# Kernel optimization log

Measured on AMD Instinct MI355X. Metric: run time of the kernel, lower is better.

## Reference

```python
import jax, jax.numpy as jnp
import numpy as np

ITERS = 8
LAMBDA0 = 0.01
PAD = 1.0
LR = 1.0
EPS = 1e-12


def _sobel_grads(fmap):
    # kornia spatial_gradient: normalized 3x3 sobel (/8), replicate padding. fmap: C,H,W
    kx = jnp.array([[-1., 0., 1.], [-2., 0., 2.], [-1., 0., 1.]], fmap.dtype) / 8.0
    k = jnp.stack([kx, kx.T])[:, None]                       # 2,1,3,3 (OIHW)
    f = jnp.pad(fmap, ((0, 0), (1, 1), (1, 1)), mode='edge')[:, None]  # C,1,H+2,W+2
    g = jax.lax.conv_general_dilated(f, k, (1, 1), 'VALID')  # C,2,H,W
    return g[:, 0], g[:, 1]


def _bilinear(tensor, pts):
    # grid_sample bilinear, align_corners=True, at pixel coords. tensor: C,H,W; pts: N,2 (x,y) -> N,C
    c, h, w = tensor.shape
    x, y = pts[:, 0], pts[:, 1]
    x0 = jnp.clip(jnp.floor(x), 0, w - 1)
    y0 = jnp.clip(jnp.floor(y), 0, h - 1)
    x1 = jnp.clip(x0 + 1, 0, w - 1)
    y1 = jnp.clip(y0 + 1, 0, h - 1)
    wx, wy = x - x0, y - y0
    x0i, x1i = x0.astype(jnp.int32), x1.astype(jnp.int32)
    y0i, y1i = y0.astype(jnp.int32), y1.astype(jnp.int32)
    v00 = tensor[:, y0i, x0i]
    v01 = tensor[:, y0i, x1i]
    v10 = tensor[:, y1i, x0i]
    v11 = tensor[:, y1i, x1i]
    out = (v00 * (1 - wx) * (1 - wy) + v01 * wx * (1 - wy)
           + v10 * (1 - wx) * wy + v11 * wx * wy)
    return out.T


def _skew(v):
    x, y, z = v[..., 0], v[..., 1], v[..., 2]
    o = jnp.zeros_like(x)
    return jnp.stack([o, -z, y, z, o, -x, -y, x, o], -1).reshape(v.shape[:-1] + (3, 3))


def _so3exp(w):
    theta = jnp.linalg.norm(w)
    small = theta < 1e-7
    th = jnp.where(small, 1.0, theta)
    A = jnp.where(small, 1.0, jnp.sin(th) / th)
    B = jnp.where(small, 0.5, (1.0 - jnp.cos(th)) / th ** 2)
    W = _skew(w)
    return jnp.eye(3, dtype=w.dtype) + A * W + B * (W @ W)


def _normalize(x):
    return x / jnp.maximum(jnp.linalg.norm(x, axis=-1, keepdims=True), EPS)


def _pnp(p3D, feature_ref, feature_query, K, R_init, t_init):
    C, H, W = feature_query.shape
    gx, gy = _sobel_grads(feature_query)
    fref = _normalize(feature_ref)
    fx, fy, cx, cy = K[0, 0], K[1, 1], K[0, 2], K[1, 2]
    f_scale = jnp.stack([fx, fy])
    c_off = jnp.stack([cx, cy])

    def project(R, t):
        p3q = p3D @ R.T + t
        pn = p3q[:, :2] / p3q[:, 2:3]
        return p3q, pn, pn * f_scale + c_off

    def in_image(p2):
        return ((p2[:, 0] >= PAD) & (p2[:, 0] < W - PAD)
                & (p2[:, 1] >= PAD) & (p2[:, 1] < H - PAD))

    def masked_cost(p2, vf):
        f = _normalize(_bilinear(feature_query, p2))
        cost = ((f - fref) ** 2).sum(-1)
        return (cost * vf).sum() / vf.sum()

    R, t = R_init, t_init
    lam = jnp.asarray(LAMBDA0, p3D.dtype)
    jacobi = None
    cost_best = None
    p2D_init = None

    for i in range(ITERS):
        p3q, pn, p2 = project(R, t)
        if i == 0:
            p2D_init = jax.lax.stop_gradient(p2)
        vf = in_image(p2).astype(p3D.dtype)  # mask-weight == gather of valid pts

        f_raw = _bilinear(feature_query, p2)  # N,C
        norm = jnp.maximum(jnp.linalg.norm(f_raw, axis=-1, keepdims=True), EPS)
        f = f_raw / norm
        error = f - fref
        if i == 0:
            cost_best = (((error ** 2).sum(-1)) * vf).sum() / vf.sum()

        # Jacobian chain: J = J_f_p2 @ J_p2_pn @ J_pn_p3 @ J_p3_T   -> N,C,6
        x_, y_, d = p3q[:, 0], p3q[:, 1], p3q[:, 2]
        z = jnp.zeros_like(d)
        Jpn = jnp.stack([1 / d, z, -x_ / d ** 2,
                         z, 1 / d, -y_ / d ** 2], -1).reshape(-1, 2, 3)
        Jpn = Jpn * f_scale[None, :, None]  # fold in J_p2_pn = diag(fx,fy)
        Jp3T = jnp.concatenate(
            [jnp.broadcast_to(jnp.eye(3, dtype=p3D.dtype), p3q.shape[:-1] + (3, 3)),
             -_skew(p3q)], -1)  # N,3,6
        J26 = Jpn @ Jp3T       # N,2,6

        Jf = jnp.stack([_bilinear(gx, p2), _bilinear(gy, p2)], -1)  # N,C,2
        # normalize-feat Jacobian (I - f f^T)/||f_raw||, fused (no NxCxC)
        proj = jnp.einsum('nc,nck->nk', f, Jf)
        Jf = (Jf - f[:, :, None] * proj[:, None, :]) / norm[:, :, None]

        J = Jf @ J26  # N,C,6
        if i == 0:
            jacobi = 1.0 / (1.0 + jnp.linalg.norm(J * vf[:, None, None], axis=(0, 1)))
        J = J * jacobi

        Grad = jnp.einsum('ncj,nc,n->j', J, error, vf)
        Hess = jnp.einsum('nci,ncj,n->ij', J, J, vf)

        damp = jnp.diag(jnp.diagonal(Hess) + 1e-9) * lam  # LM damping
        delta = -LR * jnp.linalg.solve(Hess + damp, Grad)
        delta = delta * jacobi
        dt, dw = delta[:3], delta[3:6]
        dr = _so3exp(dw)
        R_new, t_new = dr @ R, dr @ t + dt

        _, _, p2_new = project(R_new, t_new)
        vf_new = in_image(p2_new).astype(p3D.dtype)
        cost_new = masked_cost(p2_new, vf_new)

        accept = cost_new <= cost_best
        lam = jnp.clip(lam * jnp.where(accept, 0.1, 10.0), 1e-8, 1e4)
        R = jnp.where(accept, R_new, R)
        t = jnp.where(accept, t_new, t)
        cost_best = jnp.where(accept, cost_new, cost_best)

    p3D_sg = jax.lax.stop_gradient(p3D)
    pf = p3D_sg @ R.T + t
    p2f = (pf[:, :2] / pf[:, 2:3]) * f_scale + c_off
    f_i = _normalize(_bilinear(feature_query, p2D_init))
    f_f = _normalize(_bilinear(feature_query, p2f))
    cost_init = ((fref - f_i) ** 2).sum(-1)
    cost_final = ((fref - f_f) ** 2).sum(-1)
    nan = jnp.asarray(jnp.nan, cost_init.dtype)
    cost_init = jnp.where(in_image(p2D_init), cost_init, nan)
    cost_final = jnp.where(in_image(p2f), cost_final, nan)
    return R, t, cost_init, cost_final


def setup_inputs() -> dict:
    N, C, H, W = 10000, 128, 512, 512
    key = jax.random.key(0)
    ks = jax.random.split(key, 4)
    xy = jax.random.uniform(ks[0], (N, 2), jnp.float32, -2.0, 2.0)
    z = jax.random.uniform(ks[1], (N, 1), jnp.float32, 4.0, 10.0)
    p3D = jnp.concatenate([xy, z], -1)
    feature_query = jax.random.normal(ks[2], (C, H, W), jnp.float32) * 0.5
    feature_ref = jax.random.normal(ks[3], (N, C), jnp.float32)
    K = jnp.array([[500., 0., 256.], [0., 500., 256.], [0., 0., 1.]], jnp.float32)
    R_init = _so3exp(jnp.array([0.01, -0.02, 0.015], jnp.float32))
    t_init = jnp.array([0.05, -0.03, 0.10], jnp.float32)
    return {"p3D": p3D, "feature_ref": feature_ref, "feature_query": feature_query,
            "K": K, "R_init": R_init, "t_init": t_init}


def reference(p3D, feature_ref, feature_query, K, R_init, t_init):
    return _pnp(p3D, feature_ref, feature_query, K, R_init, t_init)
```

## Files before the change

### kernel.cpp

```cpp
#include <hip/hip_runtime.h>
#include <hip/hip_fp16.h>
#include <math.h>

#define HW_ (512*512)

typedef float vf4 __attribute__((ext_vector_type(4)));

__device__ __forceinline__ float wred(float v){
#pragma unroll
  for (int o = 32; o > 0; o >>= 1) v += __shfl_xor(v, o, 64);
  return v;
}

template<bool TR>
__device__ __forceinline__ float2 tap(const void* __restrict__ f, int y, int x, int c0){
  if (TR){
    const __half2* p = (const __half2*)f + (((size_t)((y << 9) + x)) << 6) + (c0 >> 1);
    return __half22float2(*p);
  } else {
    const float* ff = (const float*)f;
    int base = (y << 9) + x;
    float2 r;
    r.x = ff[(size_t)c0 * HW_ + base];
    r.y = ff[(size_t)(c0 + 1) * HW_ + base];
    return r;
  }
}

template<bool TR>
__device__ __forceinline__ float cost_point_raw(const void* __restrict__ fmap,
                                                const float* __restrict__ fref,
                                                int n, float px, float py, int lane){
  int c0 = 2 * lane;
  float x0f = fminf(fmaxf(floorf(px), 0.f), 511.f);
  float y0f = fminf(fmaxf(floorf(py), 0.f), 511.f);
  int x0 = (int)x0f, y0 = (int)y0f;
  int x1 = min(x0 + 1, 511), y1 = min(y0 + 1, 511);
  float wx = px - x0f, wy = py - y0f;
  float w00 = (1.f-wx)*(1.f-wy), w01 = wx*(1.f-wy), w10 = (1.f-wx)*wy, w11 = wx*wy;
  float2 a = tap<TR>(fmap, y0, x0, c0), b = tap<TR>(fmap, y0, x1, c0);
  float2 c = tap<TR>(fmap, y1, x0, c0), d = tap<TR>(fmap, y1, x1, c0);
  float f0 = w00*a.x + w01*b.x + w10*c.x + w11*d.x;
  float f1 = w00*a.y + w01*b.y + w10*c.y + w11*d.y;
  const float2 fr = *(const float2*)(fref + (size_t)n*128 + c0);
  float Sff  = wred(f0*f0 + f1*f1);
  float Sffr = wred(f0*fr.x + f1*fr.y);
  float Sfr  = wred(fr.x*fr.x + fr.y*fr.y);
  float inv = 1.f / fmaxf(sqrtf(Sff), 1e-12f);
  float irn = 1.f / fmaxf(sqrtf(Sfr), 1e-12f);
  return Sff*inv*inv - 2.f*Sffr*inv*irn + Sfr*irn*irn;
}

__global__ __launch_bounds__(512) void transpose_kernel(const float* __restrict__ fq,
                                                        __half* __restrict__ ftr,
                                                        double* __restrict__ cur2){
  __shared__ __half tile[256 * 128];
  int t = threadIdx.x;
  if (blockIdx.x == 0 && t < 256) cur2[t] = 0.0;
  int sb = blockIdx.x << 8;
  int l = t & 63, r = t >> 6;
  int px0 = l << 2;
#pragma unroll
  for (int p = 0; p < 16; p++){
    int ch = p * 8 + r;
    vf4 v = __builtin_nontemporal_load((const vf4*)(fq + (size_t)ch * HW_ + sb + px0));
#pragma unroll
    for (int j = 0; j < 4; j++){
      int px = px0 + j;
      tile[px * 128 + (ch ^ (px & 0x78))] = __float2half(v[j]);
    }
  }
  __syncthreads();
#pragma unroll
  for (int p = 0; p < 8; p++){
    int px = p * 32 + (t >> 4);
    int c8 = (t & 15) << 3;
    int cs = c8 ^ (px & 0x78);
    uint4 v = *(const uint4*)&tile[px * 128 + cs];
    *(uint4*)(ftr + ((size_t)(sb + px) << 7) + c8) = v;
  }
}

__global__ void init_kernel(double* __restrict__ cur2){
  if (threadIdx.x < 256) cur2[threadIdx.x] = 0.0;
}

template<bool TR>
__device__ __forceinline__ bool gather_pt(
    const float* __restrict__ p3D, const float* __restrict__ fref,
    const void* __restrict__ fmap, const float* Rl, const float* Tl,
    float fx, float fy, float cx, float cy,
    int n, int lane, float s[10], float& X, float& Y, float& D)
{
  float PX = p3D[3*n], PY = p3D[3*n+1], PZ = p3D[3*n+2];
  X = Rl[0]*PX + Rl[1]*PY + Rl[2]*PZ + Tl[0];
  Y = Rl[3]*PX + Rl[4]*PY + Rl[5]*PZ + Tl[1];
  D = Rl[6]*PX + Rl[7]*PY + Rl[8]*PZ + Tl[2];
  float px = X / D * fx + cx;
  float py = Y / D * fy + cy;
  if (!(px >= 1.f && px < 511.f && py >= 1.f && py < 511.f)) return false;
  int c0 = 2 * lane;
  float x0f = fminf(fmaxf(floorf(px), 0.f), 511.f);
  float y0f = fminf(fmaxf(floorf(py), 0.f), 511.f);
  int x0 = (int)x0f, y0 = (int)y0f;
  int x1 = min(x0 + 1, 511), y1 = min(y0 + 1, 511);
  float wx = px - x0f, wy = py - y0f;
  int xs0 = max(x0-1,0), xs3 = min(x1+1,511);
  int ys0 = max(y0-1,0), ys3 = min(y1+1,511);
  float ea = (1.f-wx)*(1.f-wy), eb = wx*(1.f-wy), ec = (1.f-wx)*wy, ed = wx*wy;
  float a8 = 0.125f*ea, b8 = 0.125f*eb, c8 = 0.125f*ec, d8 = 0.125f*ed;
  float gL1 = 2.f*a8 + c8, gR1 = 2.f*b8 + d8;
  float gL2 = a8 + 2.f*c8, gR2 = b8 + 2.f*d8;
  float ya0 = a8, ya1 = 2.f*a8 + b8, ya2 = a8 + 2.f*b8, ya3 = b8;
  float yc0 = c8, yc1 = 2.f*c8 + d8, yc2 = c8 + 2.f*d8, yc3 = d8;
  float f0=0.f, f1=0.f, gx0=0.f, gx1=0.f, gy0=0.f, gy1=0.f;
  float2 t0, t1, t2, t3;
  t0 = tap<TR>(fmap, ys0, xs0, c0); t1 = tap<TR>(fmap, ys0, x0, c0);
  t2 = tap<TR>(fmap, ys0, x1,  c0); t3 = tap<TR>(fmap, ys0, xs3, c0);
  gx0 += a8*(t2.x-t0.x) + b8*(t3.x-t1.x);
  gx1 += a8*(t2.y-t0.y) + b8*(t3.y-t1.y);
  gy0 -= ya0*t0.x + ya1*t1.x + ya2*t2.x + ya3*t3.x;
  gy1 -= ya0*t0.y + ya1*t1.y + ya2*t2.y + ya3*t3.y;
  t0 = tap<TR>(fmap, y0, xs0, c0); t1 = tap<TR>(fmap, y0, x0, c0);
  t2 = tap<TR>(fmap, y0, x1,  c0); t3 = tap<TR>(fmap, y0, xs3, c0);
  gx0 += gL1*(t2.x-t0.x) + gR1*(t3.x-t1.x);
  gx1 += gL1*(t2.y-t0.y) + gR1*(t3.y-t1.y);
  gy0 -= yc0*t0.x + yc1*t1.x + yc2*t2.x + yc3*t3.x;
  gy1 -= yc0*t0.y + yc1*t1.y + yc2*t2.y + yc3*t3.y;
  f0 += ea*t1.x + eb*t2.x;  f1 += ea*t1.y + eb*t2.y;
  t0 = tap<TR>(fmap, y1, xs0, c0); t1 = tap<TR>(fmap, y1, x0, c0);
  t2 = tap<TR>(fmap, y1, x1,  c0); t3 = tap<TR>(fmap, y1, xs3, c0);
  gx0 += gL2*(t2.x-t0.x) + gR2*(t3.x-t1.x);
  gx1 += gL2*(t2.y-t0.y) + gR2*(t3.y-t1.y);
  gy0 += ya0*t0.x + ya1*t1.x + ya2*t2.x + ya3*t3.x;
  gy1 += ya0*t0.y + ya1*t1.y + ya2*t2.y + ya3*t3.y;
  f0 += ec*t1.x + ed*t2.x;  f1 += ec*t1.y + ed*t2.y;
  t0 = tap<TR>(fmap, ys3, xs0, c0); t1 = tap<TR>(fmap, ys3, x0, c0);
  t2 = tap<TR>(fmap, ys3, x1,  c0); t3 = tap<TR>(fmap, ys3, xs3, c0);
  gx0 += c8*(t2.x-t0.x) + d8*(t3.x-t1.x);
  gx1 += c8*(t2.y-t0.y) + d8*(t3.y-t1.y);
  gy0 += yc0*t0.x + yc1*t1.x + yc2*t2.x + yc3*t3.x;
  gy1 += yc0*t0.y + yc1*t1.y + yc2*t2.y + yc3*t3.y;
  const float2 fr = *(const float2*)(fref + (size_t)n*128 + c0);
  s[0] = f0*f0 + f1*f1;
  s[1] = f0*fr.x + f1*fr.y;
  s[2] = fr.x*fr.x + fr.y*fr.y;
  s[3] = f0*gx0 + f1*gx1;
  s[4] = f0*gy0 + f1*gy1;
  s[5] = gx0*fr.x + gx1*fr.y;
  s[6] = gy0*fr.x + gy1*fr.y;
  s[7] = gx0*gx0 + gx1*gx1;
  s[8] = gx0*gy0 + gx1*gy1;
  s[9] = gy0*gy0 + gy1*gy1;
  return true;
}

__device__ __forceinline__ float slot_val(const float s[10], float X, float Y, float D,
                                          float fx, float fy, int lane, int li, int lj,
                                          float& se2)
{
  float inv = 1.f / fmaxf(sqrtf(s[0]), 1e-12f);
  float irn = 1.f / fmaxf(sqrtf(s[2]), 1e-12f);
  float inv2 = inv*inv, inv3 = inv2*inv, inv4 = inv2*inv2;
  float Sffr = s[1]*irn, Sgxfr = s[5]*irn, Sgyfr = s[6]*irn, Sfr = s[2]*irn*irn;
  se2 = s[0]*inv2 - 2.f*Sffr*inv + Sfr;
  float gex = s[3]*inv2 - Sgxfr*inv - s[3]*s[0]*inv4 + s[3]*Sffr*inv3;
  float gey = s[4]*inv2 - Sgyfr*inv - s[4]*s[0]*inv4 + s[4]*Sffr*inv3;
  float sxx = s[7]*inv2 - s[3]*s[3]*inv4;
  float sxy = s[8]*inv2 - s[3]*s[4]*inv4;
  float syy = s[9]*inv2 - s[4]*s[4]*inv4;
  float invD = 1.f / D;
  float rx = X * invD, ry = Y * invD;
  float A[6] = {fx*invD, 0.f, -fx*rx*invD, -fx*rx*ry, fx*(1.f+rx*rx), -fx*ry};
  float B[6] = {0.f, fy*invD, -fy*ry*invD, -fy*(1.f+ry*ry), fy*rx*ry, fy*rx};
  float val = 0.f;
  if (lane < 6)        val = A[lane]*gex + B[lane]*gey;
  else if (lane < 27)  val = A[li]*A[lj]*sxx + (A[li]*B[lj] + A[lj]*B[li])*sxy + B[li]*B[lj]*syy;
  else if (lane == 27) val = se2;
  else if (lane == 28) val = 1.f;
  return val;
}

template<bool TR>
__global__ __launch_bounds__(256) void eval_kernel(
    const float* __restrict__ p3D, const float* __restrict__ fref,
    const void* __restrict__ fmap, const float* __restrict__ Km,
    const float* __restrict__ Rm, const float* __restrict__ tm,
    const float* __restrict__ state, double* __restrict__ cur2,
    float* __restrict__ costT, float* __restrict__ costF,
    float* __restrict__ costI, int N, int mode)
{
  int t = threadIdx.x, lane = t & 63, wv = t >> 6;
  int gw = blockIdx.x * 4 + wv;
  int nw = (gridDim.x * blockDim.x) >> 6;
  if (mode == 1 && state[32] != 0.f){
    int nn = gw + lane * nw;
    if (lane < 4 && nn < N) costF[nn] = costT[nn];
  }
  float fx = Km[0], fy = Km[4], cx = Km[2], cy = Km[5];
  float Rl[9], Tl[3];
#pragma unroll
  for (int i = 0; i < 9; i++) Rl[i] = Rm[i];
#pragma unroll
  for (int i = 0; i < 3; i++) Tl[i] = tm[i];
  int li = 0, lj = 0;
  {
    const int pi_[21] = {0,0,0,0,0,0,1,1,1,1,1,2,2,2,2,3,3,3,4,4,5};
    const int pj_[21] = {0,1,2,3,4,5,1,2,3,4,5,2,3,4,5,3,4,5,4,5,5};
    if (lane >= 6 && lane < 27){ li = pi_[lane-6]; lj = pj_[lane-6]; }
  }
  const float nanv = __int_as_float(0x7fc00000);
  double acc = 0.0;
  for (int n = gw; n < N; n += nw){
    float s[10], X, Y, D;
    bool v = gather_pt<TR>(p3D, fref, fmap, Rl, Tl, fx, fy, cx, cy, n, lane, s, X, Y, D);
    float se2 = 0.f;
    if (v){
#pragma unroll
      for (int i = 0; i < 10; i++) s[i] = wred(s[i]);
      acc += (double)slot_val(s, X, Y, D, fx, fy, lane, li, lj, se2);
    }
    if (lane == 0){
      float cv = v ? se2 : nanv;
      if (mode == 0){ costI[n] = cv; costF[n] = cv; }
      else costT[n] = cv;
    }
  }
  __shared__ double red[4][32];
  if (lane < 32) red[wv][lane] = acc;
  __syncthreads();
  if (t < 32){
    double ssum = red[0][t] + red[1][t] + red[2][t] + red[3][t];
    if (ssum != 0.0) atomicAdd(&cur2[t*8 + (blockIdx.x & 7)], ssum);
  }
}

template<bool TR>
__global__ __launch_bounds__(256) void cost_kernel(
    const float* __restrict__ p3D, const float* __restrict__ fref,
    const void* __restrict__ fmap, const float* __restrict__ Km,
    const float* __restrict__ Rm, const float* __restrict__ tm,
    const float* __restrict__ state, double* __restrict__ cur2,
    float* __restrict__ costT, float* __restrict__ costF, int N)
{
  int t = threadIdx.x, lane = t & 63, wv = t >> 6;
  int gw = blockIdx.x * 4 + wv;
  int nw = (gridDim.x * blockDim.x) >> 6;
  if (state[32] != 0.f){
    int nn = gw + lane * nw;
    if (lane < 4 && nn < N) costF[nn] = costT[nn];
  }
  float fx = Km[0], fy = Km[4], cx = Km[2], cy = Km[5];
  float Rl[9], Tl[3];
#pragma unroll
  for (int i = 0; i < 9; i++) Rl[i] = Rm[i];
#pragma unroll
  for (int i = 0; i < 3; i++) Tl[i] = tm[i];
  const float nanv = __int_as_float(0x7fc00000);
  double accc = 0.0, accn = 0.0;
  for (int n = gw; n < N; n += nw){
    float PX = p3D[3*n], PY = p3D[3*n+1], PZ = p3D[3*n+2];
    float X = Rl[0]*PX + Rl[1]*PY + Rl[2]*PZ + Tl[0];
    float Y = Rl[3]*PX + Rl[4]*PY + Rl[5]*PZ + Tl[1];
    float D = Rl[6]*PX + Rl[7]*PY + Rl[8]*PZ + Tl[2];
    float px = X / D * fx + cx, py = Y / D * fy + cy;
    bool v = (px >= 1.f && px < 511.f && py >= 1.f && py < 511.f);
    float cp = 0.f;
    if (v){ cp = cost_point_raw<TR>(fmap, fref, n, px, py, lane); accc += (double)cp; accn += 1.0; }
    if (lane == 0) costT[n] = v ? cp : nanv;
  }
  double acc = (lane == 27) ? accc : ((lane == 28) ? accn : 0.0);
  __shared__ double red[4][32];
  if (lane < 32) red[wv][lane] = acc;
  __syncthreads();
  if (t < 32){
    double ssum = red[0][t] + red[1][t] + red[2][t] + red[3][t];
    if (ssum != 0.0) atomicAdd(&cur2[t*8 + (blockIdx.x & 7)], ssum);
  }
}

__device__ void solve_step(const double* __restrict__ cur, float* __restrict__ state){
  const int pi_[21] = {0,0,0,0,0,0,1,1,1,1,1,2,2,2,2,3,3,3,4,4,5};
  const int pj_[21] = {0,1,2,3,4,5,1,2,3,4,5,2,3,4,5,3,4,5,4,5,5};
  double rg[6]; for (int i = 0; i < 6; i++) rg[i] = cur[i];
  double rh[6][6];
  for (int k = 0; k < 21; k++){ rh[pi_[k]][pj_[k]] = cur[6+k]; rh[pj_[k]][pi_[k]] = cur[6+k]; }
  float jac[6];
  for (int j = 0; j < 6; j++) jac[j] = state[24+j];
  double lam = (double)state[30];
  double H[6][7];
  for (int i = 0; i < 6; i++)
    for (int j = 0; j < 6; j++) H[i][j] = (double)jac[i] * (double)jac[j] * rh[i][j];
  for (int i = 0; i < 6; i++) H[i][i] += (H[i][i] + 1e-9) * lam;
  for (int i = 0; i < 6; i++) H[i][6] = -((double)jac[i] * rg[i]);
  for (int k = 0; k < 6; k++){
    int p = k; double mx = fabs(H[k][k]);
    for (int r = k+1; r < 6; r++) if (fabs(H[r][k]) > mx){ mx = fabs(H[r][k]); p = r; }
    if (p != k) for (int c = k; c < 7; c++){ double tmp = H[k][c]; H[k][c] = H[p][c]; H[p][c] = tmp; }
    double inv = 1.0 / H[k][k];
    for (int r = k+1; r < 6; r++){
      double m = H[r][k] * inv;
      for (int c = k; c < 7; c++) H[r][c] -= m * H[k][c];
    }
  }
  double d[6];
  for (int i = 5; i >= 0; i--){
    double sx = H[i][6];
    for (int c = i+1; c < 6; c++) sx -= H[i][c] * d[c];
    d[i] = sx / H[i][i];
  }
  for (int j = 0; j < 6; j++) d[j] *= (double)jac[j];
  double wx = d[3], wy = d[4], wz = d[5];
  double th2 = wx*wx + wy*wy + wz*wz, th = sqrt(th2);
  double Aa, Bb;
  if (th < 1e-7){ Aa = 1.0; Bb = 0.5; } else { Aa = sin(th)/th; Bb = (1.0 - cos(th))/th2; }
  double W[3][3] = {{0,-wz,wy},{wz,0,-wx},{-wy,wx,0}};
  double W2[3][3];
  for (int i = 0; i < 3; i++) for (int j = 0; j < 3; j++){
    double q = 0; for (int k = 0; k < 3; k++) q += W[i][k]*W[k][j]; W2[i][j] = q;
  }
  double dr[3][3];
  for (int i = 0; i < 3; i++) for (int j = 0; j < 3; j++)
    dr[i][j] = (i == j ? 1.0 : 0.0) + Aa*W[i][j] + Bb*W2[i][j];
  double Rc[3][3], tc[3];
  for (int i = 0; i < 3; i++){ tc[i] = state[9+i]; for (int j = 0; j < 3; j++) Rc[i][j] = state[i*3+j]; }
  for (int i = 0; i < 3; i++){
    for (int j = 0; j < 3; j++){
      double q = 0; for (int k = 0; k < 3; k++) q += dr[i][k]*Rc[k][j];
      state[12 + i*3 + j] = (float)q;
    }
    double q = 0; for (int k = 0; k < 3; k++) q += dr[i][k]*tc[k];
    state[21 + i] = (float)(q + d[i]);
  }
}

__global__ void update_kernel(double* __restrict__ cur2, float* __restrict__ state,
                              double* __restrict__ cur,
                              const float* __restrict__ Rin, const float* __restrict__ tin,
                              int iter)
{
  __shared__ double tot[32];
  int t = threadIdx.x;
  if (t < 32){
    double s = 0.0;
#pragma unroll
    for (int k = 0; k < 8; k++){ s += cur2[t*8 + k]; cur2[t*8 + k] = 0.0; }
    tot[t] = s;
  }
  __syncthreads();
  if (t != 0) return;
  if (iter < 0){
    for (int i = 0; i < 9; i++) state[i] = Rin[i];
    for (int i = 0; i < 3; i++) state[9+i] = tin[i];
    state[30] = 0.01f;
    state[32] = 0.f;
    const int diag_k[6] = {0, 6, 11, 15, 18, 20};
    for (int j = 0; j < 6; j++)
      state[24+j] = 1.0f / (1.0f + (float)sqrt(tot[6 + diag_k[j]]));
    state[31] = (float)(tot[27] / tot[28]);
    for (int k = 0; k < 32; k++) cur[k] = tot[k];
    solve_step(cur, state);
  } else {
    float cn = (float)(tot[27] / tot[28]);
    bool acpt = (cn <= state[31]);
    float lam = state[30] * (acpt ? 0.1f : 10.f);
    state[30] = fminf(fmaxf(lam, 1e-8f), 1e4f);
    state[32] = acpt ? 1.f : 0.f;
    if (acpt){
      for (int i = 0; i < 12; i++) state[i] = state[12+i];
      state[31] = cn;
      for (int k = 0; k < 32; k++) cur[k] = tot[k];
    }
    if (iter < 7) solve_step(cur, state);
  }
}

__global__ __launch_bounds__(256) void final_kernel(const float* __restrict__ state,
                                                    const float* __restrict__ costT,
                                                    float* __restrict__ out, int N)
{
  int g = blockIdx.x * blockDim.x + threadIdx.x;
  if (g < 12) out[g] = state[g];
  if (state[32] != 0.f){
    int stride = gridDim.x * blockDim.x;
    for (int n = g; n < N; n += stride) out[12 + N + n] = costT[n];
  }
}

extern "C" void kernel_launch(void* const* d_in, const int* in_sizes, int n_in,
                              void* d_out, int out_size, void* d_ws, size_t ws_size,
                              hipStream_t stream)
{
  const float* p3D  = (const float*)d_in[0];
  const float* fref = (const float*)d_in[1];
  const float* fq   = (const float*)d_in[2];
  const float* Km   = (const float*)d_in[3];
  const float* Rin  = (const float*)d_in[4];
  const float* tin  = (const float*)d_in[5];
  float* out = (float*)d_out;
  int N = in_sizes[0] / 3;
  const int EBLK = 1024;

  char* w = (char*)d_ws;
  float*  state = (float*)w;
  double* cur   = (double*)(w + 256);
  double* cur2  = (double*)(w + 512);
  float*  costT = (float*)(w + 2560);
  size_t ftr_off = (2560 + (size_t)N*4 + 255) & ~(size_t)255;
  __half* ftr = (__half*)(w + ftr_off);
  size_t need = ftr_off + (size_t)HW_ * 128 * 2;
  bool tr = (ws_size >= need);

  float* costI = out + 12;
  float* costF = out + 12 + N;

  if (tr) transpose_kernel<<<HW_/256, 512, 0, stream>>>(fq, ftr, cur2);
  else    init_kernel<<<1, 256, 0, stream>>>(cur2);
  const void* fmap = tr ? (const void*)ftr : (const void*)fq;

  if (tr) eval_kernel<true ><<<EBLK, 256, 0, stream>>>(p3D, fref, fmap, Km, Rin, tin, state, cur2, costT, costF, costI, N, 0);
  else    eval_kernel<false><<<EBLK, 256, 0, stream>>>(p3D, fref, fmap, Km, Rin, tin, state, cur2, costT, costF, costI, N, 0);
  update_kernel<<<1, 64, 0, stream>>>(cur2, state, cur, Rin, tin, -1);

  for (int it = 0; it < 7; it++){
    if (tr) eval_kernel<true ><<<EBLK, 256, 0, stream>>>(p3D, fref, fmap, Km, state + 12, state + 21, state, cur2, costT, costF, nullptr, N, 1);
    else    eval_kernel<false><<<EBLK, 256, 0, stream>>>(p3D, fref, fmap, Km, state + 12, state + 21, state, cur2, costT, costF, nullptr, N, 1);
    update_kernel<<<1, 64, 0, stream>>>(cur2, state, cur, Rin, tin, it);
  }
  if (tr) cost_kernel<true ><<<EBLK, 256, 0, stream>>>(p3D, fref, fmap, Km, state + 12, state + 21, state, cur2, costT, costF, N);
  else    cost_kernel<false><<<EBLK, 256, 0, stream>>>(p3D, fref, fmap, Km, state + 12, state + 21, state, cur2, costT, costF, N);
  update_kernel<<<1, 64, 0, stream>>>(cur2, state, cur, Rin, tin, 7);

  final_kernel<<<256, 256, 0, stream>>>(state, costT, out, N);
}
```

Before: 533.4 us.

## Map one wavefront per point with 512-thread blocks and batch 4x4 tap loads

The eval and cost kernels now launch one wavefront per 3D point with 8 waves per block, replacing the grid-stride loop over 1024 blocks. The 16 neighbourhood taps are loaded into register arrays up front, and the Sobel gradient plus bilinear value are computed from that patch. The goal is more memory parallelism, since all gathers can be issued before any arithmetic, and better load balance. In exchange, each iteration launches many more blocks, doing more atomic adds into the reduction slots, and register pressure rises from holding 32 tap values.

```diff
diff --git a/kernel.cpp b/kernel.cpp
--- a/kernel.cpp
+++ b/kernel.cpp
@@ -25,6 +25,21 @@
     r.y = ff[(size_t)(c0 + 1) * HW_ + base];
     return r;
   }
+}
+
+__device__ __forceinline__ void fgrad(const float P[16], float w00, float w01, float w10, float w11,
+                                      float& f, float& gx, float& gy){
+  f = w00*P[5] + w01*P[6] + w10*P[9] + w11*P[10];
+  float gx11 = (P[2]  + 2.f*P[6]  + P[10] - P[0] - 2.f*P[4]  - P[8] ) * 0.125f;
+  float gx12 = (P[3]  + 2.f*P[7]  + P[11] - P[1] - 2.f*P[5]  - P[9] ) * 0.125f;
+  float gx21 = (P[6]  + 2.f*P[10] + P[14] - P[4] - 2.f*P[8]  - P[12]) * 0.125f;
+  float gx22 = (P[7]  + 2.f*P[11] + P[15] - P[5] - 2.f*P[9]  - P[13]) * 0.125f;
+  gx = w00*gx11 + w01*gx12 + w10*gx21 + w11*gx22;
+  float gy11 = (P[8]  + 2.f*P[9]  + P[10] - P[0] - 2.f*P[1]  - P[2] ) * 0.125f;
+  float gy12 = (P[9]  + 2.f*P[10] + P[11] - P[1] - 2.f*P[2]  - P[3] ) * 0.125f;
+  float gy21 = (P[12] + 2.f*P[13] + P[14] - P[4] - 2.f*P[5]  - P[6] ) * 0.125f;
+  float gy22 = (P[13] + 2.f*P[14] + P[15] - P[5] - 2.f*P[6]  - P[7] ) * 0.125f;
+  gy = w00*gy11 + w01*gy12 + w10*gy21 + w11*gy22;
 }
 
 template<bool TR>
@@ -86,103 +101,7 @@
 }
 
 template<bool TR>
-__device__ __forceinline__ bool gather_pt(
-    const float* __restrict__ p3D, const float* __restrict__ fref,
-    const void* __restrict__ fmap, const float* Rl, const float* Tl,
-    float fx, float fy, float cx, float cy,
-    int n, int lane, float s[10], float& X, float& Y, float& D)
-{
-  float PX = p3D[3*n], PY = p3D[3*n+1], PZ = p3D[3*n+2];
-  X = Rl[0]*PX + Rl[1]*PY + Rl[2]*PZ + Tl[0];
-  Y = Rl[3]*PX + Rl[4]*PY + Rl[5]*PZ + Tl[1];
-  D = Rl[6]*PX + Rl[7]*PY + Rl[8]*PZ + Tl[2];
-  float px = X / D * fx + cx;
-  float py = Y / D * fy + cy;
-  if (!(px >= 1.f && px < 511.f && py >= 1.f && py < 511.f)) return false;
-  int c0 = 2 * lane;
-  float x0f = fminf(fmaxf(floorf(px), 0.f), 511.f);
-  float y0f = fminf(fmaxf(floorf(py), 0.f), 511.f);
-  int x0 = (int)x0f, y0 = (int)y0f;
-  int x1 = min(x0 + 1, 511), y1 = min(y0 + 1, 511);
-  float wx = px - x0f, wy = py - y0f;
-  int xs0 = max(x0-1,0), xs3 = min(x1+1,511);
-  int ys0 = max(y0-1,0), ys3 = min(y1+1,511);
-  float ea = (1.f-wx)*(1.f-wy), eb = wx*(1.f-wy), ec = (1.f-wx)*wy, ed = wx*wy;
-  float a8 = 0.125f*ea, b8 = 0.125f*eb, c8 = 0.125f*ec, d8 = 0.125f*ed;
-  float gL1 = 2.f*a8 + c8, gR1 = 2.f*b8 + d8;
-  float gL2 = a8 + 2.f*c8, gR2 = b8 + 2.f*d8;
-  float ya0 = a8, ya1 = 2.f*a8 + b8, ya2 = a8 + 2.f*b8, ya3 = b8;
-  float yc0 = c8, yc1 = 2.f*c8 + d8, yc2 = c8 + 2.f*d8, yc3 = d8;
-  float f0=0.f, f1=0.f, gx0=0.f, gx1=0.f, gy0=0.f, gy1=0.f;
-  float2 t0, t1, t2, t3;
-  t0 = tap<TR>(fmap, ys0, xs0, c0); t1 = tap<TR>(fmap, ys0, x0, c0);
-  t2 = tap<TR>(fmap, ys0, x1,  c0); t3 = tap<TR>(fmap, ys0, xs3, c0);
-  gx0 += a8*(t2.x-t0.x) + b8*(t3.x-t1.x);
-  gx1 += a8*(t2.y-t0.y) + b8*(t3.y-t1.y);
-  gy0 -= ya0*t0.x + ya1*t1.x + ya2*t2.x + ya3*t3.x;
-  gy1 -= ya0*t0.y + ya1*t1.y + ya2*t2.y + ya3*t3.y;
-  t0 = tap<TR>(fmap, y0, xs0, c0); t1 = tap<TR>(fmap, y0, x0, c0);
-  t2 = tap<TR>(fmap, y0, x1,  c0); t3 = tap<TR>(fmap, y0, xs3, c0);
-  gx0 += gL1*(t2.x-t0.x) + gR1*(t3.x-t1.x);
-  gx1 += gL1*(t2.y-t0.y) + gR1*(t3.y-t1.y);
-  gy0 -= yc0*t0.x + yc1*t1.x + yc2*t2.x + yc3*t3.x;
-  gy1 -= yc0*t0.y + yc1*t1.y + yc2*t2.y + yc3*t3.y;
-  f0 += ea*t1.x + eb*t2.x;  f1 += ea*t1.y + eb*t2.y;
-  t0 = tap<TR>(fmap, y1, xs0, c0); t1 = tap<TR>(fmap, y1, x0, c0);
-  t2 = tap<TR>(fmap, y1, x1,  c0); t3 = tap<TR>(fmap, y1, xs3, c0);
-  gx0 += gL2*(t2.x-t0.x) + gR2*(t3.x-t1.x);
-  gx1 += gL2*(t2.y-t0.y) + gR2*(t3.y-t1.y);
-  gy0 += ya0*t0.x + ya1*t1.x + ya2*t2.x + ya3*t3.x;
-  gy1 += ya0*t0.y + ya1*t1.y + ya2*t2.y + ya3*t3.y;
-  f0 += ec*t1.x + ed*t2.x;  f1 += ec*t1.y + ed*t2.y;
-  t0 = tap<TR>(fmap, ys3, xs0, c0); t1 = tap<TR>(fmap, ys3, x0, c0);
-  t2 = tap<TR>(fmap, ys3, x1,  c0); t3 = tap<TR>(fmap, ys3, xs3, c0);
-  gx0 += c8*(t2.x-t0.x) + d8*(t3.x-t1.x);
-  gx1 += c8*(t2.y-t0.y) + d8*(t3.y-t1.y);
-  gy0 += yc0*t0.x + yc1*t1.x + yc2*t2.x + yc3*t3.x;
-  gy1 += yc0*t0.y + yc1*t1.y + yc2*t2.y + yc3*t3.y;
-  const float2 fr = *(const float2*)(fref + (size_t)n*128 + c0);
-  s[0] = f0*f0 + f1*f1;
-  s[1] = f0*fr.x + f1*fr.y;
-  s[2] = fr.x*fr.x + fr.y*fr.y;
-  s[3] = f0*gx0 + f1*gx1;
-  s[4] = f0*gy0 + f1*gy1;
-  s[5] = gx0*fr.x + gx1*fr.y;
-  s[6] = gy0*fr.x + gy1*fr.y;
-  s[7] = gx0*gx0 + gx1*gx1;
-  s[8] = gx0*gy0 + gx1*gy1;
-  s[9] = gy0*gy0 + gy1*gy1;
-  return true;
-}
-
-__device__ __forceinline__ float slot_val(const float s[10], float X, float Y, float D,
-                                          float fx, float fy, int lane, int li, int lj,
-                                          float& se2)
-{
-  float inv = 1.f / fmaxf(sqrtf(s[0]), 1e-12f);
-  float irn = 1.f / fmaxf(sqrtf(s[2]), 1e-12f);
-  float inv2 = inv*inv, inv3 = inv2*inv, inv4 = inv2*inv2;
-  float Sffr = s[1]*irn, Sgxfr = s[5]*irn, Sgyfr = s[6]*irn, Sfr = s[2]*irn*irn;
-  se2 = s[0]*inv2 - 2.f*Sffr*inv + Sfr;
-  float gex = s[3]*inv2 - Sgxfr*inv - s[3]*s[0]*inv4 + s[3]*Sffr*inv3;
-  float gey = s[4]*inv2 - Sgyfr*inv - s[4]*s[0]*inv4 + s[4]*Sffr*inv3;
-  float sxx = s[7]*inv2 - s[3]*s[3]*inv4;
-  float sxy = s[8]*inv2 - s[3]*s[4]*inv4;
-  float syy = s[9]*inv2 - s[4]*s[4]*inv4;
-  float invD = 1.f / D;
-  float rx = X * invD, ry = Y * invD;
-  float A[6] = {fx*invD, 0.f, -fx*rx*invD, -fx*rx*ry, fx*(1.f+rx*rx), -fx*ry};
-  float B[6] = {0.f, fy*invD, -fy*ry*invD, -fy*(1.f+ry*ry), fy*rx*ry, fy*rx};
-  float val = 0.f;
-  if (lane < 6)        val = A[lane]*gex + B[lane]*gey;
-  else if (lane < 27)  val = A[li]*A[lj]*sxx + (A[li]*B[lj] + A[lj]*B[li])*sxy + B[li]*B[lj]*syy;
-  else if (lane == 27) val = se2;
-  else if (lane == 28) val = 1.f;
-  return val;
-}
-
-template<bool TR>
-__global__ __launch_bounds__(256) void eval_kernel(
+__global__ __launch_bounds__(512) void eval_kernel(
     const float* __restrict__ p3D, const float* __restrict__ fref,
     const void* __restrict__ fmap, const float* __restrict__ Km,
     const float* __restrict__ Rm, const float* __restrict__ tm,
@@ -190,92 +109,146 @@
     float* __restrict__ costT, float* __restrict__ costF,
     float* __restrict__ costI, int N, int mode)
 {
-  int t = threadIdx.x, lane = t & 63, wv = t >> 6;
-  int gw = blockIdx.x * 4 + wv;
-  int nw = (gridDim.x * blockDim.x) >> 6;
+  int t = threadIdx.x;
+  int lane = t & 63;
+  int wv = t >> 6;
+  int n = blockIdx.x * 8 + wv;
   if (mode == 1 && state[32] != 0.f){
-    int nn = gw + lane * nw;
-    if (lane < 4 && nn < N) costF[nn] = costT[nn];
-  }
-  float fx = Km[0], fy = Km[4], cx = Km[2], cy = Km[5];
-  float Rl[9], Tl[3];
-#pragma unroll
-  for (int i = 0; i < 9; i++) Rl[i] = Rm[i];
-#pragma unroll
-  for (int i = 0; i < 3; i++) Tl[i] = tm[i];
-  int li = 0, lj = 0;
-  {
-    const int pi_[21] = {0,0,0,0,0,0,1,1,1,1,1,2,2,2,2,3,3,3,4,4,5};
-    const int pj_[21] = {0,1,2,3,4,5,1,2,3,4,5,2,3,4,5,3,4,5,4,5,5};
-    if (lane >= 6 && lane < 27){ li = pi_[lane-6]; lj = pj_[lane-6]; }
-  }
-  const float nanv = __int_as_float(0x7fc00000);
+    int gid = blockIdx.x * 512 + t;
+    if (gid < N) costF[gid] = costT[gid];
+  }
   double acc = 0.0;
-  for (int n = gw; n < N; n += nw){
-    float s[10], X, Y, D;
-    bool v = gather_pt<TR>(p3D, fref, fmap, Rl, Tl, fx, fy, cx, cy, n, lane, s, X, Y, D);
+  if (n < N){
+    float fx = Km[0], fy = Km[4], cx = Km[2], cy = Km[5];
+    float R0=Rm[0],R1=Rm[1],R2=Rm[2],R3=Rm[3],R4=Rm[4];
+    float R5=Rm[5],R6=Rm[6],R7=Rm[7],R8=Rm[8];
+    float t0=tm[0], t1=tm[1], t2=tm[2];
+    float PX = p3D[3*n], PY = p3D[3*n+1], PZ = p3D[3*n+2];
+    float X = R0*PX + R1*PY + R2*PZ + t0;
+    float Y = R3*PX + R4*PY + R5*PZ + t1;
+    float D = R6*PX + R7*PY + R8*PZ + t2;
+    float px = X / D * fx + cx;
+    float py = Y / D * fy + cy;
+    bool valid = (px >= 1.f && px < 511.f && py >= 1.f && py < 511.f);
     float se2 = 0.f;
-    if (v){
-#pragma unroll
-      for (int i = 0; i < 10; i++) s[i] = wred(s[i]);
-      acc += (double)slot_val(s, X, Y, D, fx, fy, lane, li, lj, se2);
+    if (valid){
+      int c0 = 2 * lane;
+      float x0f = fminf(fmaxf(floorf(px), 0.f), 511.f);
+      float y0f = fminf(fmaxf(floorf(py), 0.f), 511.f);
+      int x0 = (int)x0f, y0 = (int)y0f;
+      int x1 = min(x0 + 1, 511), y1 = min(y0 + 1, 511);
+      float wx = px - x0f, wy = py - y0f;
+      int xs[4] = {max(x0-1,0), x0, x1, min(x1+1,511)};
+      int ys[4] = {max(y0-1,0), y0, y1, min(y1+1,511)};
+      float Pa[16], Pb[16];
+#pragma unroll
+      for (int r = 0; r < 4; r++)
+#pragma unroll
+        for (int sc = 0; sc < 4; sc++){
+          float2 v = tap<TR>(fmap, ys[r], xs[sc], c0);
+          Pa[r*4+sc] = v.x; Pb[r*4+sc] = v.y;
+        }
+      float w00 = (1.f-wx)*(1.f-wy), w01 = wx*(1.f-wy), w10 = (1.f-wx)*wy, w11 = wx*wy;
+      float f0, gx0, gy0, f1, gx1, gy1;
+      fgrad(Pa, w00, w01, w10, w11, f0, gx0, gy0);
+      fgrad(Pb, w00, w01, w10, w11, f1, gx1, gy1);
+      const float2 fr2 = *(const float2*)(fref + (size_t)n*128 + c0);
+      float Sff   = wred(f0*f0   + f1*f1);
+      float Sffr0 = wred(f0*fr2.x + f1*fr2.y);
+      float Sfr   = wred(fr2.x*fr2.x + fr2.y*fr2.y);
+      float Sfgx  = wred(f0*gx0  + f1*gx1);
+      float Sfgy  = wred(f0*gy0  + f1*gy1);
+      float Sgxf0 = wred(gx0*fr2.x + gx1*fr2.y);
+      float Sgyf0 = wred(gy0*fr2.x + gy1*fr2.y);
+      float Sgxgx = wred(gx0*gx0 + gx1*gx1);
+      float Sgxgy = wred(gx0*gy0 + gx1*gy1);
+      float Sgygy = wred(gy0*gy0 + gy1*gy1);
+      float irn = 1.f / fmaxf(sqrtf(Sfr), 1e-12f);
+      float Sffr = Sffr0*irn, Sgxfr = Sgxf0*irn, Sgyfr = Sgyf0*irn, Sfrn = Sfr*irn*irn;
+      float nrm = fmaxf(sqrtf(Sff), 1e-12f);
+      float inv = 1.f/nrm, inv2 = inv*inv, inv3 = inv2*inv, inv4 = inv2*inv2;
+      se2 = Sff*inv2 - 2.f*Sffr*inv + Sfrn;
+      float gex = Sfgx*inv2 - Sgxfr*inv - Sfgx*Sff*inv4 + Sfgx*Sffr*inv3;
+      float gey = Sfgy*inv2 - Sgyfr*inv - Sfgy*Sff*inv4 + Sfgy*Sffr*inv3;
+      float sxx = Sgxgx*inv2 - Sfgx*Sfgx*inv4;
+      float sxy = Sgxgy*inv2 - Sfgx*Sfgy*inv4;
+      float syy = Sgygy*inv2 - Sfgy*Sfgy*inv4;
+      float invD = 1.f / D;
+      float rx = X * invD, ry = Y * invD;
+      float A[6] = {fx*invD, 0.f, -fx*rx*invD, -fx*rx*ry, fx*(1.f+rx*rx), -fx*ry};
+      float B[6] = {0.f, fy*invD, -fy*ry*invD, -fy*(1.f+ry*ry), fy*rx*ry, fy*rx};
+      int li = 0, lj = 0;
+      {
+        const int pi_[21] = {0,0,0,0,0,0,1,1,1,1,1,2,2,2,2,3,3,3,4,4,5};
+        const int pj_[21] = {0,1,2,3,4,5,1,2,3,4,5,2,3,4,5,3,4,5,4,5,5};
+        if (lane >= 6 && lane < 27){ li = pi_[lane-6]; lj = pj_[lane-6]; }
+      }
+      float val = 0.f;
+      if (lane < 6)        val = A[lane]*gex + B[lane]*gey;
+      else if (lane < 27)  val = A[li]*A[lj]*sxx + (A[li]*B[lj] + A[lj]*B[li])*sxy + B[li]*B[lj]*syy;
+      else if (lane == 27) val = se2;
+      else if (lane == 28) val = 1.f;
+      acc = (double)val;
     }
     if (lane == 0){
-      float cv = v ? se2 : nanv;
+      float cv = valid ? se2 : __int_as_float(0x7fc00000);
       if (mode == 0){ costI[n] = cv; costF[n] = cv; }
       else costT[n] = cv;
     }
   }
-  __shared__ double red[4][32];
+  __shared__ double red[8][32];
   if (lane < 32) red[wv][lane] = acc;
   __syncthreads();
   if (t < 32){
-    double ssum = red[0][t] + red[1][t] + red[2][t] + red[3][t];
-    if (ssum != 0.0) atomicAdd(&cur2[t*8 + (blockIdx.x & 7)], ssum);
+    double s = 0.0;
+#pragma unroll
+    for (int i = 0; i < 8; i++) s += red[i][t];
+    if (s != 0.0) atomicAdd(&cur2[t*8 + (blockIdx.x & 7)], s);
   }
 }
 
 template<bool TR>
-__global__ __launch_bounds__(256) void cost_kernel(
+__global__ __launch_bounds__(512) void cost_kernel(
     const float* __restrict__ p3D, const float* __restrict__ fref,
     const void* __restrict__ fmap, const float* __restrict__ Km,
     const float* __restrict__ Rm, const float* __restrict__ tm,
     const float* __restrict__ state, double* __restrict__ cur2,
     float* __restrict__ costT, float* __restrict__ costF, int N)
 {
-  int t = threadIdx.x, lane = t & 63, wv = t >> 6;
-  int gw = blockIdx.x * 4 + wv;
-  int nw = (gridDim.x * blockDim.x) >> 6;
+  int t = threadIdx.x;
+  int lane = t & 63;
+  int wv = t >> 6;
+  int n = blockIdx.x * 8 + wv;
   if (state[32] != 0.f){
-    int nn = gw + lane * nw;
-    if (lane < 4 && nn < N) costF[nn] = costT[nn];
-  }
-  float fx = Km[0], fy = Km[4], cx = Km[2], cy = Km[5];
-  float Rl[9], Tl[3];
-#pragma unroll
-  for (int i = 0; i < 9; i++) Rl[i] = Rm[i];
-#pragma unroll
-  for (int i = 0; i < 3; i++) Tl[i] = tm[i];
-  const float nanv = __int_as_float(0x7fc00000);
-  double accc = 0.0, accn = 0.0;
-  for (int n = gw; n < N; n += nw){
+    int gid = blockIdx.x * 512 + t;
+    if (gid < N) costF[gid] = costT[gid];
+  }
+  double acc = 0.0;
+  bool valid = false;
+  float cp = 0.f;
+  if (n < N){
+    float fx = Km[0], fy = Km[4], cx = Km[2], cy = Km[5];
     float PX = p3D[3*n], PY = p3D[3*n+1], PZ = p3D[3*n+2];
-    float X = Rl[0]*PX + Rl[1]*PY + Rl[2]*PZ + Tl[0];
-    float Y = Rl[3]*PX + Rl[4]*PY + Rl[5]*PZ + Tl[1];
-    float D = Rl[6]*PX + Rl[7]*PY + Rl[8]*PZ + Tl[2];
+    float X = Rm[0]*PX + Rm[1]*PY + Rm[2]*PZ + tm[0];
+    float Y = Rm[3]*PX + Rm[4]*PY + Rm[5]*PZ + tm[1];
+    float D = Rm[6]*PX + Rm[7]*PY + Rm[8]*PZ + tm[2];
     float px = X / D * fx + cx, py = Y / D * fy + cy;
-    bool v = (px >= 1.f && px < 511.f && py >= 1.f && py < 511.f);
-    float cp = 0.f;
-    if (v){ cp = cost_point_raw<TR>(fmap, fref, n, px, py, lane); accc += (double)cp; accn += 1.0; }
-    if (lane == 0) costT[n] = v ? cp : nanv;
-  }
-  double acc = (lane == 27) ? accc : ((lane == 28) ? accn : 0.0);
-  __shared__ double red[4][32];
+    valid = (px >= 1.f && px < 511.f && py >= 1.f && py < 511.f);
+    if (valid) cp = cost_point_raw<TR>(fmap, fref, n, px, py, lane);
+    if (lane == 0) costT[n] = valid ? cp : __int_as_float(0x7fc00000);
+    if (valid){
+      if (lane == 27) acc = (double)cp;
+      else if (lane == 28) acc = 1.0;
+    }
+  }
+  __shared__ double red[8][32];
   if (lane < 32) red[wv][lane] = acc;
   __syncthreads();
   if (t < 32){
-    double ssum = red[0][t] + red[1][t] + red[2][t] + red[3][t];
-    if (ssum != 0.0) atomicAdd(&cur2[t*8 + (blockIdx.x & 7)], ssum);
+    double s = 0.0;
+#pragma unroll
+    for (int i = 0; i < 8; i++) s += red[i][t];
+    if (s != 0.0) atomicAdd(&cur2[t*8 + (blockIdx.x & 7)], s);
   }
 }
 
@@ -399,7 +372,7 @@
   const float* tin  = (const float*)d_in[5];
   float* out = (float*)d_out;
   int N = in_sizes[0] / 3;
-  const int EBLK = 1024;
+  int NBLK = (N + 7) / 8;
 
   char* w = (char*)d_ws;
   float*  state = (float*)w;
@@ -418,17 +391,17 @@
   else    init_kernel<<<1, 256, 0, stream>>>(cur2);
   const void* fmap = tr ? (const void*)ftr : (const void*)fq;
 
-  if (tr) eval_kernel<true ><<<EBLK, 256, 0, stream>>>(p3D, fref, fmap, Km, Rin, tin, state, cur2, costT, costF, costI, N, 0);
-  else    eval_kernel<false><<<EBLK, 256, 0, stream>>>(p3D, fref, fmap, Km, Rin, tin, state, cur2, costT, costF, costI, N, 0);
+  if (tr) eval_kernel<true ><<<NBLK, 512, 0, stream>>>(p3D, fref, fmap, Km, Rin, tin, state, cur2, costT, costF, costI, N, 0);
+  else    eval_kernel<false><<<NBLK, 512, 0, stream>>>(p3D, fref, fmap, Km, Rin, tin, state, cur2, costT, costF, costI, N, 0);
   update_kernel<<<1, 64, 0, stream>>>(cur2, state, cur, Rin, tin, -1);
 
   for (int it = 0; it < 7; it++){
-    if (tr) eval_kernel<true ><<<EBLK, 256, 0, stream>>>(p3D, fref, fmap, Km, state + 12, state + 21, state, cur2, costT, costF, nullptr, N, 1);
-    else    eval_kernel<false><<<EBLK, 256, 0, stream>>>(p3D, fref, fmap, Km, state + 12, state + 21, state, cur2, costT, costF, nullptr, N, 1);
+    if (tr) eval_kernel<true ><<<NBLK, 512, 0, stream>>>(p3D, fref, fmap, Km, state + 12, state + 21, state, cur2, costT, costF, nullptr, N, 1);
+    else    eval_kernel<false><<<NBLK, 512, 0, stream>>>(p3D, fref, fmap, Km, state + 12, state + 21, state, cur2, costT, costF, nullptr, N, 1);
     update_kernel<<<1, 64, 0, stream>>>(cur2, state, cur, Rin, tin, it);
   }
-  if (tr) cost_kernel<true ><<<EBLK, 256, 0, stream>>>(p3D, fref, fmap, Km, state + 12, state + 21, state, cur2, costT, costF, N);
-  else    cost_kernel<false><<<EBLK, 256, 0, stream>>>(p3D, fref, fmap, Km, state + 12, state + 21, state, cur2, costT, costF, N);
+  if (tr) cost_kernel<true ><<<NBLK, 512, 0, stream>>>(p3D, fref, fmap, Km, state + 12, state + 21, state, cur2, costT, costF, N);
+  else    cost_kernel<false><<<NBLK, 512, 0, stream>>>(p3D, fref, fmap, Km, state + 12, state + 21, state, cur2, costT, costF, N);
   update_kernel<<<1, 64, 0, stream>>>(cur2, state, cur, Rin, tin, 7);
 
   final_kernel<<<256, 256, 0, stream>>>(state, costT, out, N);
```

Measured after the change: 553.6 us. 1.04x slower.
